# Kernel tuning notes

Hardware: AMD Instinct MI355X
Metric: run time of the kernel (lower is better)

The kernel has to match this reference:

```python
import jax, jax.numpy as jnp
import numpy as np


def setup_inputs() -> dict:
    key = jax.random.key(0)
    ks = jax.random.split(key, 4)
    B, T, C, L, DQ = 8, 2048, 256, 32, 512
    return {
        "vis_feats": jax.random.normal(ks[0], (B, T, C), dtype=jnp.float32),
        "query": jax.random.normal(ks[1], (B, L, DQ), dtype=jnp.float32),
        "W1": jax.random.normal(ks[2], (DQ, C), dtype=jnp.float32) / np.float32(np.sqrt(DQ)),
        "b1": jnp.zeros((C,), dtype=jnp.float32),
        "W2": jax.random.normal(ks[3], (DQ, C), dtype=jnp.float32) / np.float32(np.sqrt(DQ)),
        "b2": jnp.zeros((C,), dtype=jnp.float32),
        "window_size": 32,
        "num_chunks": 8,
    }


def reference(vis_feats, query, W1, b1, W2, b2, window_size, num_chunks):
    B, T, C = vis_feats.shape
    L = query.shape[1]
    # seq encoders (modeled as linear projections): [B, L, C]
    enc1 = query @ W1 + b1
    enc2 = query @ W2 + b2
    # clip-word similarity and per-clip word label: [B, T]
    sim = jnp.einsum("btc,blc->btl", vis_feats, enc1)
    clip_labels = jnp.argmax(sim, axis=2)
    NW = T - window_size + 1
    cic = window_size // num_chunks  # clips per chunk
    # sliding-window unfold indices: [NW, window_size]
    idx = jnp.arange(NW)[:, None] + jnp.arange(window_size)[None, :]
    vis_unf = vis_feats[:, idx, :]                      # [B, NW, W, C]
    lab_unf = clip_labels[:, idx].reshape(B, NW, num_chunks, cic)
    # majority vote per chunk == argmax of label histogram (ties -> smallest label,
    # matching np.bincount + np.argmax)
    counts = jax.nn.one_hot(lab_unf, L, dtype=jnp.int32).sum(axis=3)  # [B, NW, K, L]
    lbls = jnp.argmax(counts, axis=-1)                  # [B, NW, K]
    # adaptive_avg_pool3d (K, cic, C) -> (K, 1, C) == mean over clips-in-chunk
    pooled = vis_unf.reshape(B, NW, num_chunks, cic, C).mean(axis=3)  # [B, NW, K, C]
    # gather the majority-vote word encoding and modulate
    gathered = enc2[jnp.arange(B)[:, None, None], lbls]  # [B, NW, K, C]
    return gathered * pooled
```

## Files before the change

kernel.cpp:

```cpp
#include <hip/hip_runtime.h>
#include <hip/hip_bf16.h>

#define B   8
#define T   2048
#define C   256
#define L   32
#define DQ  512
#define NW  2017
#define NK  8
#define CIC 4
#define WT  32
#define SROWS (WT + (NK-1)*CIC)

__global__ __launch_bounds__(1024) void enc_kernel(
    const float* __restrict__ query, const float* __restrict__ W1,
    const float* __restrict__ b1, const float* __restrict__ W2,
    const float* __restrict__ b2, float* __restrict__ enc1,
    float* __restrict__ enc2) {
  const int b = blockIdx.y, lg = blockIdx.x;
  const int c = threadIdx.x;
  const int q = threadIdx.y;
  __shared__ float qs[4 * DQ];
  __shared__ float red[2][4][4][256];
  const float* qbase = query + ((size_t)b * L + lg * 4) * DQ;
  for (int i = q * 256 + c; i < 4 * DQ; i += 1024) qs[i] = qbase[i];
  __syncthreads();
  float a1[4] = {0.f, 0.f, 0.f, 0.f};
  float a2[4] = {0.f, 0.f, 0.f, 0.f};
  const int d0 = q * (DQ / 4);
#pragma unroll 4
  for (int dd = 0; dd < DQ / 4; ++dd) {
    const int d = d0 + dd;
    const float w1 = W1[d * C + c];
    const float w2 = W2[d * C + c];
#pragma unroll
    for (int j = 0; j < 4; ++j) {
      a1[j] = fmaf(qs[j * DQ + d], w1, a1[j]);
      a2[j] = fmaf(qs[j * DQ + d], w2, a2[j]);
    }
  }
#pragma unroll
  for (int j = 0; j < 4; ++j) {
    red[0][q][j][c] = a1[j];
    red[1][q][j][c] = a2[j];
  }
  __syncthreads();
  for (int o = q * 256 + c; o < 2048; o += 1024) {
    const int e = o >> 10;
    const int j = (o >> 8) & 3;
    const int cc = o & 255;
    const float v = red[e][0][j][cc] + red[e][1][j][cc] +
                    red[e][2][j][cc] + red[e][3][j][cc];
    const size_t off = ((size_t)b * L + lg * 4 + j) * C + cc;
    if (e == 0) enc1[off] = v + b1[cc];
    else        enc2[off] = v + b2[cc];
  }
}

__global__ __launch_bounds__(256) void label_kernel(
    const float* __restrict__ vis, const float* __restrict__ enc1,
    int* __restrict__ labels) {
  const int b = blockIdx.y;
  const int t0 = blockIdx.x * 32;
  const int tid = threadIdx.x;
  const int tl = tid & 31;
  const int part = tid >> 5;
  __shared__ float4 e1[L * (C / 4)];
  __shared__ float pacc[32][8 * L + 1];
  const float4* esrc = (const float4*)(enc1 + (size_t)b * L * C);
  for (int i = tid; i < L * (C / 4); i += 256) e1[i] = esrc[i];
  __syncthreads();

  const float4* vrow = (const float4*)(vis + ((size_t)b * T + t0 + tl) * C);
  float acc[L];
#pragma unroll
  for (int l = 0; l < L; ++l) acc[l] = 0.f;
  const int c4b = part * 8;
#pragma unroll
  for (int j = 0; j < 8; ++j) {
    const float4 v = vrow[c4b + j];
#pragma unroll
    for (int l = 0; l < L; ++l) {
      const float4 e = e1[l * 64 + c4b + j];
      acc[l] = fmaf(v.x, e.x, fmaf(v.y, e.y, fmaf(v.z, e.z, fmaf(v.w, e.w, acc[l]))));
    }
  }
#pragma unroll
  for (int l = 0; l < L; ++l) pacc[tl][part * L + l] = acc[l];
  __syncthreads();
  if (tid < 32) {
    float bv = -INFINITY;
    int bi = 0;
#pragma unroll
    for (int l = 0; l < L; ++l) {
      float s = 0.f;
#pragma unroll
      for (int p = 0; p < 8; ++p) s += pacc[tid][p * L + l];
      if (s > bv) { bv = s; bi = l; }
    }
    labels[(size_t)b * T + t0 + tid] = bi;
  }
}

__global__ __launch_bounds__(256) void out_kernel(
    const float* __restrict__ vis, const float* __restrict__ enc2,
    const int* __restrict__ labels, float* __restrict__ out) {
  const int b = blockIdx.y;
  const int w0 = blockIdx.x * WT;
  const int tid = threadIdx.x;
  const int lane = tid & 63;
  const int part = tid >> 6;
  __shared__ float4 S4[SROWS * (C / 4)];
  __shared__ int slbl[SROWS];

  const float4* vb = (const float4*)(vis + (size_t)b * T * C);
  {
    const int s_begin = part * (SROWS / 4);
    float4 r[18];
#pragma unroll
    for (int j = 0; j < 18; ++j) {
      int t = w0 + s_begin + j;
      t = t > (T - 1) ? (T - 1) : t;
      r[j] = vb[(size_t)t * (C / 4) + lane];
    }
#pragma unroll
    for (int s = 0; s < SROWS / 4; ++s) {
      float4 sum;
      sum.x = (r[s].x + r[s + 1].x + r[s + 2].x + r[s + 3].x) * 0.25f;
      sum.y = (r[s].y + r[s + 1].y + r[s + 2].y + r[s + 3].y) * 0.25f;
      sum.z = (r[s].z + r[s + 1].z + r[s + 2].z + r[s + 3].z) * 0.25f;
      sum.w = (r[s].w + r[s + 1].w + r[s + 2].w + r[s + 3].w) * 0.25f;
      S4[(s_begin + s) * (C / 4) + lane] = sum;
    }
  }

  if (tid < SROWS) {
    const int* lb = labels + (size_t)b * T;
    const int t = w0 + tid;
#define LCL(tt) lb[(tt) > (T - 1) ? (T - 1) : (tt)]
    const int l0 = LCL(t), l1 = LCL(t + 1), l2 = LCL(t + 2), l3 = LCL(t + 3);
#undef LCL
    const int c0 = 1 + (l0 == l1) + (l0 == l2) + (l0 == l3);
    const int c1 = 1 + (l1 == l0) + (l1 == l2) + (l1 == l3);
    const int c2 = 1 + (l2 == l0) + (l2 == l1) + (l2 == l3);
    const int c3 = 1 + (l3 == l0) + (l3 == l1) + (l3 == l2);
    int best = l0, bc = c0;
    if (c1 > bc || (c1 == bc && l1 < best)) { best = l1; bc = c1; }
    if (c2 > bc || (c2 == bc && l2 < best)) { best = l2; bc = c2; }
    if (c3 > bc || (c3 == bc && l3 < best)) { best = l3; bc = c3; }
    slbl[tid] = best;
  }
  __syncthreads();

  const float4* e2b = (const float4*)(enc2 + (size_t)b * L * C);
  float4* outp = (float4*)out;
  const int wlim = (NW - w0) < WT ? (NW - w0) : WT;
#pragma unroll
  for (int kk = 0; kk < 2; ++kk) {
    const int k = part + kk * 4;
#pragma unroll 4
    for (int w = 0; w < wlim; ++w) {
      const int s = w + CIC * k;
      const int lbl = slbl[s];
      const float4 e = e2b[lbl * (C / 4) + lane];
      const float4 sv = S4[s * (C / 4) + lane];
      float4 o;
      o.x = e.x * sv.x; o.y = e.y * sv.y; o.z = e.z * sv.z; o.w = e.w * sv.w;
      outp[(((size_t)b * NW + w0 + w) * NK + k) * (C / 4) + lane] = o;
    }
  }
}

extern "C" void kernel_launch(void* const* d_in, const int* in_sizes, int n_in,
                              void* d_out, int out_size, void* d_ws, size_t ws_size,
                              hipStream_t stream) {
  const float* vis   = (const float*)d_in[0];
  const float* query = (const float*)d_in[1];
  const float* W1    = (const float*)d_in[2];
  const float* b1    = (const float*)d_in[3];
  const float* W2    = (const float*)d_in[4];
  const float* b2    = (const float*)d_in[5];
  float* out = (float*)d_out;

  float* enc1 = (float*)d_ws;
  float* enc2 = enc1 + (size_t)B * L * C;
  int* labels = (int*)(enc2 + (size_t)B * L * C);

  enc_kernel<<<dim3(L / 4, B), dim3(256, 4), 0, stream>>>(query, W1, b1, W2, b2, enc1, enc2);
  label_kernel<<<dim3(T / 32, B), 256, 0, stream>>>(vis, enc1, labels);
  out_kernel<<<dim3((NW + WT - 1) / WT, B), 256, 0, stream>>>(vis, enc2, labels, out);
}
```

Baseline: 217.9 us.

## Fuse label computation into output kernel with shared vis tile

Merges the label and output kernels into one. Each block loads its window of vis rows (63 rows) into shared memory once, computes per-clip argmax labels from that tile with enc1 held in registers, then does the chunk pooling and the enc2 gather in place. This removes one kernel launch, the labels round trip through global memory, and the second read of vis. In exchange, overlapping blocks recompute labels for about twice as many rows, the serial 63-iteration dot loop adds latency, and shared memory use grows.

```diff
diff --git a/kernel.cpp b/kernel.cpp
--- a/kernel.cpp
+++ b/kernel.cpp
@@ -11,6 +11,7 @@
 #define CIC 4
 #define WT  32
 #define SROWS (WT + (NK-1)*CIC)
+#define RROWS (WT - 1 + 32)
 
 __global__ __launch_bounds__(1024) void enc_kernel(
     const float* __restrict__ query, const float* __restrict__ W1,
@@ -57,89 +58,64 @@
   }
 }
 
-__global__ __launch_bounds__(256) void label_kernel(
+__global__ __launch_bounds__(256) void fused_kernel(
     const float* __restrict__ vis, const float* __restrict__ enc1,
-    int* __restrict__ labels) {
+    const float* __restrict__ enc2, float* __restrict__ out) {
   const int b = blockIdx.y;
-  const int t0 = blockIdx.x * 32;
+  const int w0 = blockIdx.x * WT;
   const int tid = threadIdx.x;
-  const int tl = tid & 31;
+
+  __shared__ float4 raw[RROWS * (C / 4)];
+  __shared__ float pacc[4][RROWS][33];
+  __shared__ int tlabel[RROWS];
+  __shared__ int slbl[SROWS];
+
+  const int l = tid & 31;
   const int part = tid >> 5;
-  __shared__ float4 e1[L * (C / 4)];
-  __shared__ float pacc[32][8 * L + 1];
-  const float4* esrc = (const float4*)(enc1 + (size_t)b * L * C);
-  for (int i = tid; i < L * (C / 4); i += 256) e1[i] = esrc[i];
+  float4 ef[8];
+  {
+    const float4* e1p = (const float4*)(enc1 + ((size_t)b * L + l) * C) + part * 8;
+#pragma unroll
+    for (int j = 0; j < 8; ++j) ef[j] = e1p[j];
+  }
+
+  const float4* vb = (const float4*)(vis + (size_t)b * T * C);
+  for (int i = tid; i < RROWS * (C / 4); i += 256) {
+    int row = w0 + (i >> 6);
+    row = row > (T - 1) ? (T - 1) : row;
+    raw[i] = vb[(size_t)row * (C / 4) + (i & 63)];
+  }
   __syncthreads();
 
-  const float4* vrow = (const float4*)(vis + ((size_t)b * T + t0 + tl) * C);
-  float acc[L];
+  for (int t = 0; t < RROWS; ++t) {
+    const float4* vr = &raw[t * (C / 4) + part * 8];
+    float a = 0.f;
 #pragma unroll
-  for (int l = 0; l < L; ++l) acc[l] = 0.f;
-  const int c4b = part * 8;
-#pragma unroll
-  for (int j = 0; j < 8; ++j) {
-    const float4 v = vrow[c4b + j];
-#pragma unroll
-    for (int l = 0; l < L; ++l) {
-      const float4 e = e1[l * 64 + c4b + j];
-      acc[l] = fmaf(v.x, e.x, fmaf(v.y, e.y, fmaf(v.z, e.z, fmaf(v.w, e.w, acc[l]))));
+    for (int j = 0; j < 8; ++j) {
+      const float4 v = vr[j];
+      a = fmaf(v.x, ef[j].x, fmaf(v.y, ef[j].y, fmaf(v.z, ef[j].z, fmaf(v.w, ef[j].w, a))));
     }
+    a += __shfl_down(a, 32);
+    if (!(tid & 32)) pacc[tid >> 6][t][l] = a;
   }
-#pragma unroll
-  for (int l = 0; l < L; ++l) pacc[tl][part * L + l] = acc[l];
   __syncthreads();
-  if (tid < 32) {
+
+  if (tid < RROWS) {
     float bv = -INFINITY;
     int bi = 0;
 #pragma unroll
-    for (int l = 0; l < L; ++l) {
-      float s = 0.f;
-#pragma unroll
-      for (int p = 0; p < 8; ++p) s += pacc[tid][p * L + l];
-      if (s > bv) { bv = s; bi = l; }
+    for (int ll = 0; ll < L; ++ll) {
+      const float s = pacc[0][tid][ll] + pacc[1][tid][ll] +
+                      pacc[2][tid][ll] + pacc[3][tid][ll];
+      if (s > bv) { bv = s; bi = ll; }
     }
-    labels[(size_t)b * T + t0 + tid] = bi;
+    tlabel[tid] = bi;
   }
-}
-
-__global__ __launch_bounds__(256) void out_kernel(
-    const float* __restrict__ vis, const float* __restrict__ enc2,
-    const int* __restrict__ labels, float* __restrict__ out) {
-  const int b = blockIdx.y;
-  const int w0 = blockIdx.x * WT;
-  const int tid = threadIdx.x;
-  const int lane = tid & 63;
-  const int part = tid >> 6;
-  __shared__ float4 S4[SROWS * (C / 4)];
-  __shared__ int slbl[SROWS];
-
-  const float4* vb = (const float4*)(vis + (size_t)b * T * C);
-  {
-    const int s_begin = part * (SROWS / 4);
-    float4 r[18];
-#pragma unroll
-    for (int j = 0; j < 18; ++j) {
-      int t = w0 + s_begin + j;
-      t = t > (T - 1) ? (T - 1) : t;
-      r[j] = vb[(size_t)t * (C / 4) + lane];
-    }
-#pragma unroll
-    for (int s = 0; s < SROWS / 4; ++s) {
-      float4 sum;
-      sum.x = (r[s].x + r[s + 1].x + r[s + 2].x + r[s + 3].x) * 0.25f;
-      sum.y = (r[s].y + r[s + 1].y + r[s + 2].y + r[s + 3].y) * 0.25f;
-      sum.z = (r[s].z + r[s + 1].z + r[s + 2].z + r[s + 3].z) * 0.25f;
-      sum.w = (r[s].w + r[s + 1].w + r[s + 2].w + r[s + 3].w) * 0.25f;
-      S4[(s_begin + s) * (C / 4) + lane] = sum;
-    }
-  }
+  __syncthreads();
 
   if (tid < SROWS) {
-    const int* lb = labels + (size_t)b * T;
-    const int t = w0 + tid;
-#define LCL(tt) lb[(tt) > (T - 1) ? (T - 1) : (tt)]
-    const int l0 = LCL(t), l1 = LCL(t + 1), l2 = LCL(t + 2), l3 = LCL(t + 3);
-#undef LCL
+    const int l0 = tlabel[tid], l1 = tlabel[tid + 1];
+    const int l2 = tlabel[tid + 2], l3 = tlabel[tid + 3];
     const int c0 = 1 + (l0 == l1) + (l0 == l2) + (l0 == l3);
     const int c1 = 1 + (l1 == l0) + (l1 == l2) + (l1 == l3);
     const int c2 = 1 + (l2 == l0) + (l2 == l1) + (l2 == l3);
@@ -150,6 +126,29 @@
     if (c3 > bc || (c3 == bc && l3 < best)) { best = l3; bc = c3; }
     slbl[tid] = best;
   }
+
+  const int lane = tid & 63;
+  const int wv = tid >> 6;
+  float4 r[18];
+  {
+    const int s0 = wv * (SROWS / 4);
+#pragma unroll
+    for (int j = 0; j < 18; ++j) r[j] = raw[(s0 + j) * (C / 4) + lane];
+  }
+  __syncthreads();
+
+  {
+    const int s0 = wv * (SROWS / 4);
+#pragma unroll
+    for (int s = 0; s < SROWS / 4; ++s) {
+      float4 o;
+      o.x = (r[s].x + r[s + 1].x + r[s + 2].x + r[s + 3].x) * 0.25f;
+      o.y = (r[s].y + r[s + 1].y + r[s + 2].y + r[s + 3].y) * 0.25f;
+      o.z = (r[s].z + r[s + 1].z + r[s + 2].z + r[s + 3].z) * 0.25f;
+      o.w = (r[s].w + r[s + 1].w + r[s + 2].w + r[s + 3].w) * 0.25f;
+      raw[(s0 + s) * (C / 4) + lane] = o;
+    }
+  }
   __syncthreads();
 
   const float4* e2b = (const float4*)(enc2 + (size_t)b * L * C);
@@ -157,13 +156,13 @@
   const int wlim = (NW - w0) < WT ? (NW - w0) : WT;
 #pragma unroll
   for (int kk = 0; kk < 2; ++kk) {
-    const int k = part + kk * 4;
+    const int k = wv + kk * 4;
 #pragma unroll 4
     for (int w = 0; w < wlim; ++w) {
       const int s = w + CIC * k;
-      const int lbl = slbl[s];
-      const float4 e = e2b[lbl * (C / 4) + lane];
-      const float4 sv = S4[s * (C / 4) + lane];
+      const int lb = slbl[s];
+      const float4 e = e2b[lb * (C / 4) + lane];
+      const float4 sv = raw[s * (C / 4) + lane];
       float4 o;
       o.x = e.x * sv.x; o.y = e.y * sv.y; o.z = e.z * sv.z; o.w = e.w * sv.w;
       outp[(((size_t)b * NW + w0 + w) * NK + k) * (C / 4) + lane] = o;
@@ -184,9 +183,7 @@
 
   float* enc1 = (float*)d_ws;
   float* enc2 = enc1 + (size_t)B * L * C;
-  int* labels = (int*)(enc2 + (size_t)B * L * C);
 
   enc_kernel<<<dim3(L / 4, B), dim3(256, 4), 0, stream>>>(query, W1, b1, W2, b2, enc1, enc2);
-  label_kernel<<<dim3(T / 32, B), 256, 0, stream>>>(vis, enc1, labels);
-  out_kernel<<<dim3((NW + WT - 1) / WT, B), 256, 0, stream>>>(vis, enc2, labels, out);
+  fused_kernel<<<dim3((NW + WT - 1) / WT, B), 256, 0, stream>>>(vis, enc1, enc2, out);
 }
```

Result: slower. 240.7 us (+10.5%).
